# Optimization experiments

Measured on AMD Instinct MI355X. Metric: run time of the kernel, lower is better.

## Reference

```python
import jax, jax.numpy as jnp
import numpy as np

BETA = 0.25


def setup_inputs() -> dict:
    key = jax.random.key(0)
    k1, k2 = jax.random.split(key)
    x = jax.random.normal(k1, (32, 64, 64, 64), dtype=jnp.float32)   # [B, C, H, W]
    emb = jax.random.normal(k2, (1024, 64), dtype=jnp.float32)       # [K, C] codebook
    return {"x": x, "emb": emb}


def reference(x, emb):
    b, c, h, w = x.shape
    # (b h w) c
    z = jnp.transpose(x, (0, 2, 3, 1)).reshape(-1, c)
    # squared euclidean distances (argmin identical to torch.cdist argmin)
    # ||z||^2 - 2 z e^T + ||e||^2, never taking sqrt since only argmin is used
    d = (jnp.sum(z * z, axis=1, keepdims=True)
         - 2.0 * jnp.einsum('nc,kc->nk', z, emb)
         + jnp.sum(emb * emb, axis=1)[None, :])        # [N, K]
    idx = jnp.argmin(d, axis=1)                        # [N] int
    e = emb[idx]                                       # gather [N, C]
    e = jnp.transpose(e.reshape(b, h, w, c), (0, 3, 1, 2))  # [B, C, H, W]
    codebook_loss = jnp.mean((jax.lax.stop_gradient(x) - e) ** 2)
    commitment_loss = BETA * jnp.mean((x - jax.lax.stop_gradient(e)) ** 2)
    loss = codebook_loss + commitment_loss
    o = x + jax.lax.stop_gradient(e - x)               # straight-through
    indices = idx.reshape(b, h, w)
    return (o, loss, indices)
```

## Files before the change

### kernel.cpp

```cpp
#include <hip/hip_runtime.h>

#define BATCH   32
#define CCH     64
#define HW      4096
#define NPIX    (BATCH * HW)
#define KCODES  1024
#define NELEM   (NPIX * CCH)
#define MB      128
#define CK      64
#define MARGIN_Q 8u

typedef _Float16 f16;
typedef __attribute__((ext_vector_type(8))) _Float16 f16x8;
typedef __attribute__((ext_vector_type(4))) float    f32x4;

static __device__ __forceinline__ f32x4 mfma16(f16x8 a, f16x8 b, f32x4 c) {
    return __builtin_amdgcn_mfma_f32_16x16x32_f16(a, b, c, 0, 0, 0);
}

static __device__ __forceinline__ void dma16(void* lds, const void* g) {
    __builtin_amdgcn_global_load_lds(
        (const __attribute__((address_space(1))) unsigned int*)g,
        (__attribute__((address_space(3))) unsigned int*)lds, 16, 0, 0);
}

#define WS_EEB_F   64
#define WS_CBH_B   8192
#define WS_CBL_B   139264
#define WS_WL_U    67584

__global__ __launch_bounds__(256) void vq_prep(
    const float* __restrict__ emb, float* __restrict__ wsf,
    unsigned* __restrict__ wsu, f16* __restrict__ cbH, f16* __restrict__ cbL,
    float* __restrict__ eeb_g)
{
    const int t = threadIdx.x;
    if (blockIdx.x < 32) {
        const int gid = blockIdx.x * 256 + t;
        const int row = gid >> 3, gi = gid & 7;
        const float* src = emb + (size_t)row * CCH + gi * 8;
        float4 v0 = *(const float4*)(src);
        float4 v1 = *(const float4*)(src + 4);
        float vv[8] = {v0.x, v0.y, v0.z, v0.w, v1.x, v1.y, v1.z, v1.w};
        f16x8 h, l;
#pragma unroll
        for (int j = 0; j < 8; ++j) {
            f16 hh = (f16)vv[j];
            h[j] = hh;
            l[j] = (f16)(vv[j] - (float)hh);
        }
        const int off = row * 64 + 8 * (gi ^ (row & 7));
        *(f16x8*)(cbH + off) = h;
        *(f16x8*)(cbL + off) = l;
    } else {
        if (t == 0) { wsf[0] = 0.f; wsu[1] = 0u; }
        for (int r = t * 4; r < t * 4 + 4; ++r) {
            const float4* row4 = (const float4*)(emb + (size_t)r * CCH);
            float s = 0.f;
#pragma unroll
            for (int i = 0; i < 16; ++i) {
                float4 v = row4[i];
                s = fmaf(v.x, v.x, s); s = fmaf(v.y, v.y, s);
                s = fmaf(v.z, v.z, s); s = fmaf(v.w, v.w, s);
            }
            eeb_g[r] = fmaf(s, 2048.0f, 1048576.0f);
        }
    }
}

__global__ __launch_bounds__(256, 4) void vq_main(
    const float* __restrict__ x,
    const float* __restrict__ emb,
    const f16* __restrict__ cbH, const f16* __restrict__ cbL,
    const float* __restrict__ eeb_g,
    float* __restrict__ o, float* __restrict__ idx_out,
    float* __restrict__ acc, unsigned* __restrict__ wl_count,
    unsigned* __restrict__ wl, unsigned cap)
{
    __shared__ __align__(16) char smem[32768];
    __shared__ float eebl[2][CK];
    __shared__ unsigned bu1[MB], bu2[MB];
    __shared__ float wred[4];

    const int t    = threadIdx.x;
    const int lane = t & 63;
    const int w    = t >> 6;
    const int col  = lane & 15;
    const int quad = lane >> 4;
    const int c7   = col & 7;
    const int sw0  = 8 * (quad ^ c7);
    const int sw1  = sw0 ^ 32;
    const int n0   = blockIdx.x * MB;
    const int b    = n0 >> 12;
    const int p0   = n0 & 4095;
    const float* xb = x + (size_t)b * (CCH * HW) + p0;

    f16* zH = (f16*)smem;
    f16* zL = (f16*)(smem + 16384);

    {
        const int pl = t & 127;
        const int g0 = (t >> 7) * 4;
#pragma unroll
        for (int i = 0; i < 4; ++i) {
            const int g = g0 + i;
            f16x8 h, l;
#pragma unroll
            for (int j = 0; j < 8; ++j) {
                float zs = -2.0f * xb[(size_t)(g * 8 + j) * HW + pl];
                f16 hh = (f16)zs;
                h[j] = hh;
                l[j] = (f16)(zs - (float)hh);
            }
            const int off = pl * 64 + 8 * (g ^ (pl & 7));
            *(f16x8*)(zH + off) = h;
            *(f16x8*)(zL + off) = l;
        }
    }
    __syncthreads();

    f16x8 aH[2][2], aL[2][2];
#pragma unroll
    for (int rt = 0; rt < 2; ++rt) {
        const int pl = w * 32 + rt * 16 + col;
        aH[rt][0] = *(const f16x8*)&zH[pl * 64 + sw0];
        aH[rt][1] = *(const f16x8*)&zH[pl * 64 + sw1];
        aL[rt][0] = *(const f16x8*)&zL[pl * 64 + sw0];
        aL[rt][1] = *(const f16x8*)&zL[pl * 64 + sw1];
    }
    __syncthreads();

    unsigned best[8], best2[8];
#pragma unroll
    for (int s = 0; s < 8; ++s) { best[s] = 0xFFFFFFFFu; best2[s] = 0xFFFFFFFFu; }

    auto stage = [&](int chunk, int bufi) {
        const int k0 = chunk * CK;
        char* lb = smem + bufi * 16384;
        const char* gH = (const char*)cbH + (size_t)k0 * 128 + w * 2048 + lane * 16;
        const char* gL = (const char*)cbL + (size_t)k0 * 128 + w * 2048 + lane * 16;
        char* lH = lb + w * 2048;
        char* lL = lb + 8192 + w * 2048;
        dma16(lH,        gH);
        dma16(lH + 1024, gH + 1024);
        dma16(lL,        gL);
        dma16(lL + 1024, gL + 1024);
        if (t < CK) eebl[bufi][t] = eeb_g[k0 + t];
    };

    stage(0, 0);

    for (int chunk = 0; chunk < KCODES / CK; ++chunk) {
        const int cur = chunk & 1;
        __syncthreads();
        if (chunk + 1 < KCODES / CK) stage(chunk + 1, cur ^ 1);

        const f16* bufH = (const f16*)(smem + cur * 16384);
        const f16* bufL = bufH + 4096;
        const int k0 = chunk * CK;

#pragma unroll
        for (int tile = 0; tile < CK / 16; ++tile) {
            const f16* bh = bufH + (tile * 16 + col) * 64;
            const f16* bl = bufL + (tile * 16 + col) * 64;
            f16x8 bH0 = *(const f16x8*)(bh + sw0);
            f16x8 bH1 = *(const f16x8*)(bh + sw1);
            f16x8 bL0 = *(const f16x8*)(bl + sw0);
            f16x8 bL1 = *(const f16x8*)(bl + sw1);
            const float eebc = eebl[cur][tile * 16 + col];
            const unsigned kb = (unsigned)(k0 + tile * 16 + col);
#pragma unroll
            for (int rt = 0; rt < 2; ++rt) {
                f32x4 a4 = {0.f, 0.f, 0.f, 0.f};
                a4 = mfma16(aH[rt][0], bH0, a4);
                a4 = mfma16(aH[rt][1], bH1, a4);
                a4 = mfma16(aL[rt][0], bH0, a4);
                a4 = mfma16(aL[rt][1], bH1, a4);
                a4 = mfma16(aH[rt][0], bL0, a4);
                a4 = mfma16(aH[rt][1], bL1, a4);
#pragma unroll
                for (int r = 0; r < 4; ++r) {
                    float uf = fmaf(a4[r], 2048.0f, eebc);
                    unsigned pk = (((unsigned)uf) << 10) | kb;
                    const int s = rt * 4 + r;
                    unsigned mx = pk > best[s] ? pk : best[s];
                    best2[s] = best2[s] < mx ? best2[s] : mx;
                    best[s]  = best[s] < pk ? best[s] : pk;
                }
            }
        }
    }

#pragma unroll
    for (int d = 1; d < 16; d <<= 1) {
#pragma unroll
        for (int s = 0; s < 8; ++s) {
            unsigned ob  = __shfl_xor(best[s],  d, 64);
            unsigned ob2 = __shfl_xor(best2[s], d, 64);
            unsigned mx  = best[s] > ob ? best[s] : ob;
            unsigned mn2 = best2[s] < ob2 ? best2[s] : ob2;
            best2[s] = mn2 < mx ? mn2 : mx;
            best[s]  = best[s] < ob ? best[s] : ob;
        }
    }
    if (col == 0) {
#pragma unroll
        for (int rt = 0; rt < 2; ++rt)
#pragma unroll
            for (int r = 0; r < 4; ++r) {
                const int pl = w * 32 + rt * 16 + quad * 4 + r;
                bu1[pl] = best[rt * 4 + r];
                bu2[pl] = best2[rt * 4 + r];
            }
    }
    __syncthreads();

    if (t < MB) {
        const unsigned bu = bu1[t];
        idx_out[n0 + t] = (float)(bu & 1023u);
        const unsigned qg = (bu2[t] >> 10) - (bu >> 10);
        if (qg < MARGIN_Q) {
            unsigned pos = atomicAdd(wl_count, 1u);
            if (pos < cap) wl[pos] = (unsigned)(n0 + t);
        }
    }
    float ss = 0.f;
    {
        const int pl = t & 127, cs = t >> 7;
        const unsigned bidx = bu1[pl] & 1023u;
        const float* er = emb + (size_t)bidx * CCH;
        float* ob = o + (size_t)b * (CCH * HW) + p0 + pl;
        for (int c = cs; c < CCH; c += 2) {
            float xv = xb[(size_t)c * HW + pl];
            float e  = er[c];
            ob[(size_t)c * HW] = xv + (e - xv);
            float d = xv - e;
            ss = fmaf(d, d, ss);
        }
    }
    for (int off = 32; off; off >>= 1) ss += __shfl_down(ss, off, 64);
    if (lane == 0) wred[w] = ss;
    __syncthreads();
    if (t == 0) atomicAdd(acc, (wred[0] + wred[1]) + (wred[2] + wred[3]));
}

__global__ __launch_bounds__(256) void vq_refine(
    const float* __restrict__ x, const float* __restrict__ emb,
    float* __restrict__ o, float* __restrict__ idx_out,
    float* __restrict__ acc, const unsigned* __restrict__ wl_count,
    const unsigned* __restrict__ wl, unsigned cap)
{
    __shared__ float zsh[CCH];
    __shared__ double rbd[4];
    __shared__ int rbi[4];
    __shared__ int s_pk;
    unsigned cnt = *wl_count; if (cnt > cap) cnt = cap;
    const int t = threadIdx.x;

    for (unsigned i = blockIdx.x; i < cnt; i += gridDim.x) {
        const int n = (int)wl[i];
        const int b = n >> 12, p = n & 4095;
        if (t < CCH) zsh[t] = x[(size_t)b * (CCH * HW) + (size_t)t * HW + p];
        __syncthreads();

        double bd = 1e300; int bi = KCODES;
        for (int j = 0; j < 4; ++j) {
            const int k = t + j * 256;
            const float* er = emb + (size_t)k * CCH;
            double d = 0.0;
#pragma unroll
            for (int c = 0; c < CCH; ++c) {
                double tt = (double)zsh[c] - (double)er[c];
                d = fma(tt, tt, d);
            }
            if (d < bd) { bd = d; bi = k; }
        }
        for (int dlt = 1; dlt < 64; dlt <<= 1) {
            double od = __shfl_xor(bd, dlt, 64);
            int    oi = __shfl_xor(bi, dlt, 64);
            if (od < bd || (od == bd && oi < bi)) { bd = od; bi = oi; }
        }
        const int wv = t >> 6;
        if ((t & 63) == 0) { rbd[wv] = bd; rbi[wv] = bi; }
        __syncthreads();
        if (t == 0) {
            double fb = rbd[0]; int fi = rbi[0];
            for (int q = 1; q < 4; ++q)
                if (rbd[q] < fb || (rbd[q] == fb && rbi[q] < fi)) { fb = rbd[q]; fi = rbi[q]; }
            const int old = (int)idx_out[n];
            if (fi != old) { idx_out[n] = (float)fi; s_pk = (old << 16) | fi; }
            else s_pk = -1;
        }
        __syncthreads();
        const int pk = s_pk;
        if (pk >= 0 && t < CCH) {
            const int old = pk >> 16, fi = pk & 0xFFFF;
            const float xv = zsh[t];
            const float eo = emb[(size_t)old * CCH + t];
            const float en = emb[(size_t)fi  * CCH + t];
            o[(size_t)b * (CCH * HW) + (size_t)t * HW + p] = xv + (en - xv);
            const float dn = xv - en, dd = xv - eo;
            float delta = dn * dn - dd * dd;
            for (int off = 32; off; off >>= 1) delta += __shfl_down(delta, off, 64);
            if (t == 0) atomicAdd(acc, delta);
        }
        __syncthreads();
    }
}

__global__ void vq_fin(const float* __restrict__ acc, float* __restrict__ loss) {
    *loss = 1.25f * (*acc) * (1.0f / (float)NELEM);
}

extern "C" void kernel_launch(void* const* d_in, const int* in_sizes, int n_in,
                              void* d_out, int out_size, void* d_ws, size_t ws_size,
                              hipStream_t stream) {
    const float* x   = (const float*)d_in[0];
    const float* emb = (const float*)d_in[1];
    float*    out = (float*)d_out;
    float*    wsf = (float*)d_ws;
    unsigned* wsu = (unsigned*)d_ws;
    char*     wsb = (char*)d_ws;

    float* o_out    = out;
    float* loss_out = out + NELEM;
    float* idx_out  = out + NELEM + 1;
    float* eeb_g    = wsf + WS_EEB_F;
    f16*   cbH      = (f16*)(wsb + WS_CBH_B);
    f16*   cbL      = (f16*)(wsb + WS_CBL_B);
    unsigned* wl    = wsu + WS_WL_U;
    unsigned cap = 0;
    if (ws_size / 4 > WS_WL_U) {
        size_t c = ws_size / 4 - WS_WL_U;
        cap = (unsigned)(c > NPIX ? NPIX : c);
    }

    vq_prep<<<33, 256, 0, stream>>>(emb, wsf, wsu, cbH, cbL, eeb_g);
    vq_main<<<NPIX / MB, 256, 0, stream>>>(x, emb, cbH, cbL, eeb_g, o_out,
                                           idx_out, wsf, wsu + 1, wl, cap);
    vq_refine<<<512, 256, 0, stream>>>(x, emb, o_out, idx_out, wsf,
                                       wsu + 1, wl, cap);
    vq_fin<<<1, 1, 0, stream>>>(wsf, loss_out);
}
```

Baseline: 171.1 us.

## Double pixels per block, load A fragments directly, vectorize epilogue, tighten margin

Each block now handles 256 pixels: every wave covers 64 pixels (four row tiles), so each codebook chunk staged in LDS is reused across twice as many MFMAs. The A operands are built straight from global memory into registers, removing the LDS staging pass and its two barriers. The epilogue reads codebook rows as float4 with one thread per pixel. The refinement margin drops from 8 to 3, sending fewer near-tie pixels to the exact refine kernel. In exchange, register pressure rises (occupancy hint cut from 4 to 2 blocks), and a narrower margin risks wrong indices on near ties.

```diff
diff --git a/kernel.cpp b/kernel.cpp
--- a/kernel.cpp
+++ b/kernel.cpp
@@ -6,9 +6,9 @@
 #define NPIX    (BATCH * HW)
 #define KCODES  1024
 #define NELEM   (NPIX * CCH)
-#define MB      128
+#define MB      256
 #define CK      64
-#define MARGIN_Q 8u
+#define MARGIN_Q 3u
 
 typedef _Float16 f16;
 typedef __attribute__((ext_vector_type(8))) _Float16 f16x8;
@@ -68,7 +68,7 @@
     }
 }
 
-__global__ __launch_bounds__(256, 4) void vq_main(
+__global__ __launch_bounds__(256, 2) void vq_main(
     const float* __restrict__ x,
     const float* __restrict__ emb,
     const f16* __restrict__ cbH, const f16* __restrict__ cbL,
@@ -94,45 +94,6 @@
     const int b    = n0 >> 12;
     const int p0   = n0 & 4095;
     const float* xb = x + (size_t)b * (CCH * HW) + p0;
-
-    f16* zH = (f16*)smem;
-    f16* zL = (f16*)(smem + 16384);
-
-    {
-        const int pl = t & 127;
-        const int g0 = (t >> 7) * 4;
-#pragma unroll
-        for (int i = 0; i < 4; ++i) {
-            const int g = g0 + i;
-            f16x8 h, l;
-#pragma unroll
-            for (int j = 0; j < 8; ++j) {
-                float zs = -2.0f * xb[(size_t)(g * 8 + j) * HW + pl];
-                f16 hh = (f16)zs;
-                h[j] = hh;
-                l[j] = (f16)(zs - (float)hh);
-            }
-            const int off = pl * 64 + 8 * (g ^ (pl & 7));
-            *(f16x8*)(zH + off) = h;
-            *(f16x8*)(zL + off) = l;
-        }
-    }
-    __syncthreads();
-
-    f16x8 aH[2][2], aL[2][2];
-#pragma unroll
-    for (int rt = 0; rt < 2; ++rt) {
-        const int pl = w * 32 + rt * 16 + col;
-        aH[rt][0] = *(const f16x8*)&zH[pl * 64 + sw0];
-        aH[rt][1] = *(const f16x8*)&zH[pl * 64 + sw1];
-        aL[rt][0] = *(const f16x8*)&zL[pl * 64 + sw0];
-        aL[rt][1] = *(const f16x8*)&zL[pl * 64 + sw1];
-    }
-    __syncthreads();
-
-    unsigned best[8], best2[8];
-#pragma unroll
-    for (int s = 0; s < 8; ++s) { best[s] = 0xFFFFFFFFu; best2[s] = 0xFFFFFFFFu; }
 
     auto stage = [&](int chunk, int bufi) {
         const int k0 = chunk * CK;
@@ -150,6 +111,30 @@
 
     stage(0, 0);
 
+    f16x8 aH[4][2], aL[4][2];
+#pragma unroll
+    for (int rt = 0; rt < 4; ++rt) {
+        const int pp = w * 64 + rt * 16 + col;
+#pragma unroll
+        for (int kc = 0; kc < 2; ++kc) {
+            f16x8 h, l;
+#pragma unroll
+            for (int j = 0; j < 8; ++j) {
+                const int c = kc * 32 + quad * 8 + j;
+                float zs = -2.0f * xb[(size_t)c * HW + pp];
+                f16 hh = (f16)zs;
+                h[j] = hh;
+                l[j] = (f16)(zs - (float)hh);
+            }
+            aH[rt][kc] = h;
+            aL[rt][kc] = l;
+        }
+    }
+
+    unsigned best[16], best2[16];
+#pragma unroll
+    for (int s = 0; s < 16; ++s) { best[s] = 0xFFFFFFFFu; best2[s] = 0xFFFFFFFFu; }
+
     for (int chunk = 0; chunk < KCODES / CK; ++chunk) {
         const int cur = chunk & 1;
         __syncthreads();
@@ -170,7 +155,7 @@
             const float eebc = eebl[cur][tile * 16 + col];
             const unsigned kb = (unsigned)(k0 + tile * 16 + col);
 #pragma unroll
-            for (int rt = 0; rt < 2; ++rt) {
+            for (int rt = 0; rt < 4; ++rt) {
                 f32x4 a4 = {0.f, 0.f, 0.f, 0.f};
                 a4 = mfma16(aH[rt][0], bH0, a4);
                 a4 = mfma16(aH[rt][1], bH1, a4);
@@ -183,9 +168,8 @@
                     float uf = fmaf(a4[r], 2048.0f, eebc);
                     unsigned pk = (((unsigned)uf) << 10) | kb;
                     const int s = rt * 4 + r;
-                    unsigned mx = pk > best[s] ? pk : best[s];
-                    best2[s] = best2[s] < mx ? best2[s] : mx;
-                    best[s]  = best[s] < pk ? best[s] : pk;
+                    best2[s] = min(best2[s], max(pk, best[s]));
+                    best[s]  = min(best[s], pk);
                 }
             }
         }
@@ -194,30 +178,29 @@
 #pragma unroll
     for (int d = 1; d < 16; d <<= 1) {
 #pragma unroll
-        for (int s = 0; s < 8; ++s) {
+        for (int s = 0; s < 16; ++s) {
             unsigned ob  = __shfl_xor(best[s],  d, 64);
             unsigned ob2 = __shfl_xor(best2[s], d, 64);
-            unsigned mx  = best[s] > ob ? best[s] : ob;
-            unsigned mn2 = best2[s] < ob2 ? best2[s] : ob2;
-            best2[s] = mn2 < mx ? mn2 : mx;
-            best[s]  = best[s] < ob ? best[s] : ob;
+            best2[s] = min(min(best2[s], ob2), max(best[s], ob));
+            best[s]  = min(best[s], ob);
         }
     }
     if (col == 0) {
 #pragma unroll
-        for (int rt = 0; rt < 2; ++rt)
+        for (int rt = 0; rt < 4; ++rt)
 #pragma unroll
             for (int r = 0; r < 4; ++r) {
-                const int pl = w * 32 + rt * 16 + quad * 4 + r;
+                const int pl = w * 64 + rt * 16 + quad * 4 + r;
                 bu1[pl] = best[rt * 4 + r];
                 bu2[pl] = best2[rt * 4 + r];
             }
     }
     __syncthreads();
 
-    if (t < MB) {
-        const unsigned bu = bu1[t];
-        idx_out[n0 + t] = (float)(bu & 1023u);
+    const unsigned bu = bu1[t];
+    const unsigned bidx = bu & 1023u;
+    idx_out[n0 + t] = (float)bidx;
+    {
         const unsigned qg = (bu2[t] >> 10) - (bu >> 10);
         if (qg < MARGIN_Q) {
             unsigned pos = atomicAdd(wl_count, 1u);
@@ -226,16 +209,22 @@
     }
     float ss = 0.f;
     {
-        const int pl = t & 127, cs = t >> 7;
-        const unsigned bidx = bu1[pl] & 1023u;
-        const float* er = emb + (size_t)bidx * CCH;
-        float* ob = o + (size_t)b * (CCH * HW) + p0 + pl;
-        for (int c = cs; c < CCH; c += 2) {
-            float xv = xb[(size_t)c * HW + pl];
-            float e  = er[c];
-            ob[(size_t)c * HW] = xv + (e - xv);
-            float d = xv - e;
-            ss = fmaf(d, d, ss);
+        const float4* er4 = (const float4*)(emb + (size_t)bidx * CCH);
+        const float* xbt = xb + t;
+        float* ob = o + (size_t)b * (CCH * HW) + p0 + t;
+#pragma unroll
+        for (int i = 0; i < 16; ++i) {
+            float4 ev = er4[i];
+            float evv[4] = {ev.x, ev.y, ev.z, ev.w};
+#pragma unroll
+            for (int q = 0; q < 4; ++q) {
+                const int c = i * 4 + q;
+                float xv = xbt[(size_t)c * HW];
+                float e  = evv[q];
+                ob[(size_t)c * HW] = xv + (e - xv);
+                float d = xv - e;
+                ss = fmaf(d, d, ss);
+            }
         }
     }
     for (int off = 32; off; off >>= 1) ss += __shfl_down(ss, off, 64);
```

New measurement: 159.3 us. 1.07x faster.
